# Optimization experiments

Hardware: AMD Instinct MI355X
Metric: run time of the kernel (lower is better)

## Reference

```python
import jax, jax.numpy as jnp
import numpy as np


def fwht(x):
    """Fast Walsh-Hadamard transform along last axis (n must be a power of 2).
    Loop runs log2(n) times (fixed, ~12 iters) -- fully vectorized butterflies."""
    n = x.shape[-1]
    prefix = x.shape[:-1]
    x = x.reshape(-1, n)
    h = 1
    while h < n:
        x = x.reshape(-1, n // (2 * h), 2, h)
        a, b = x[:, :, 0, :], x[:, :, 1, :]
        x = jnp.stack([a + b, a - b], axis=2).reshape(-1, n)
        h *= 2
    return x.reshape(prefix + (n,))


def setup_inputs() -> dict:
    key = jax.random.key(0)
    ks = jax.random.split(key, 8)
    Bz, S, N, M = 4, 2048, 4096, 4096   # batch, seq, in_features, out_features
    CODESZ, CB_SIZE, RANK = 8, 256, 64
    inp = {}
    inp["input"] = jax.random.normal(ks[0], (Bz, S, N), dtype=jnp.float32)
    inp["Qidxs"] = jax.random.randint(ks[1], (M, N // CODESZ), 0, CB_SIZE, dtype=jnp.int32)
    inp["codebook_vals"] = jax.random.normal(ks[2], (CB_SIZE, CODESZ), dtype=jnp.float32)
    # SU/SV are random sign vectors in QuIP#
    inp["SU"] = jnp.sign(jax.random.normal(ks[3], (N,), dtype=jnp.float32))
    inp["SV"] = jnp.sign(jax.random.normal(ks[4], (M,), dtype=jnp.float32))
    inp["Wscale"] = jnp.ones((), dtype=jnp.float32)
    inp["A"] = jax.random.normal(ks[5], (M, RANK), dtype=jnp.float32) * 0.01
    inp["B"] = jax.random.normal(ks[6], (RANK, N), dtype=jnp.float32) * 0.01
    return inp


def reference(input, Qidxs, codebook_vals, SU, SV, Wscale, A, B):
    n = SU.shape[0]   # in_features
    m = SV.shape[0]   # out_features
    lead = input.shape[:-1]
    x = input.reshape(-1, n).astype(jnp.float32)          # [T, n]
    # input rotation: x <- H^T (x * SU) / sqrt(n)   (matmul_hadUt, K=1 case)
    x = fwht(x * SU) * (1.0 / jnp.sqrt(jnp.float32(n)))
    # low-rank correction branch (rank > 0)
    Bx = x @ B.T                                          # [T, rank]
    # dequantize: codebook lookup [m, n/codesz, codesz] -> [m, n]
    W = codebook_vals[Qidxs].reshape(m, n)
    z = (x @ W.T) * Wscale                                # [T, m]
    z = z + Bx @ A.T
    # output rotation: z <- SV * (H z) / sqrt(m)
    z = fwht(z) * (1.0 / jnp.sqrt(jnp.float32(m))) * SV
    return z.reshape(lead + (m,))
```

## Files before the change

kernel.cpp:

```cpp
#include <hip/hip_runtime.h>
#include <hip/hip_bf16.h>


typedef __attribute__((ext_vector_type(8))) short short8;
typedef __attribute__((ext_vector_type(16))) float f32x16;

#define T_ROWS 8192
#define NDIM   4096
#define MDIM   4096

__device__ __forceinline__ void gld_lds16(const void* g, void* lds_uniform) {
    __builtin_amdgcn_global_load_lds(
        (const __attribute__((address_space(1))) unsigned int*)(unsigned long long)(uintptr_t)g,
        (__attribute__((address_space(3))) unsigned int*)(unsigned int)(uintptr_t)lds_uniform,
        16, 0, 0);
}

__device__ __forceinline__ void bfly(float& a, float& b) {
    float s = a + b, d = a - b; a = s; b = d;
}

__device__ __forceinline__ void fwht16(float* v) {
#pragma unroll
    for (int h = 1; h <= 8; h <<= 1)
#pragma unroll
        for (int j = 0; j < 16; ++j)
            if (!(j & h)) bfly(v[j], v[j | h]);
}

__global__ __launch_bounds__(256) void fwht_in_kernel(
        const float* __restrict__ in, const float* __restrict__ SU,
        __hip_bfloat16* __restrict__ xout) {
    __shared__ float sh[4352];
    const int t = threadIdx.x;
    const size_t r = blockIdx.x;
    float v[16];
    {
        const float4* s4 = (const float4*)(in + (r << 12) + t * 16);
        const float4* u4 = (const float4*)(SU + t * 16);
#pragma unroll
        for (int q = 0; q < 4; ++q) {
            float4 a = s4[q], u = u4[q];
            v[4 * q + 0] = a.x * u.x; v[4 * q + 1] = a.y * u.y;
            v[4 * q + 2] = a.z * u.z; v[4 * q + 3] = a.w * u.w;
        }
    }
    fwht16(v);
#pragma unroll
    for (int j = 0; j < 16; ++j) sh[17 * t + j] = v[j];
    __syncthreads();
    const int baseB = (t & 15) + 272 * (t >> 4);
#pragma unroll
    for (int j = 0; j < 16; ++j) v[j] = sh[baseB + 17 * j];
    fwht16(v);
#pragma unroll
    for (int j = 0; j < 16; ++j) sh[baseB + 17 * j] = v[j];
    __syncthreads();
    const int baseC = t + (t >> 4);
#pragma unroll
    for (int j = 0; j < 16; ++j) v[j] = sh[baseC + 272 * j];
    fwht16(v);
    __hip_bfloat16* dst = xout + (r << 12);
#pragma unroll
    for (int j = 0; j < 16; ++j)
        dst[(j << 8) + t] = __float2bfloat16(v[j] * 0.015625f);
}

__global__ __launch_bounds__(256) void fwht_out_kernel(
        float* __restrict__ z, const float* __restrict__ SV) {
    __shared__ float sh[4352];
    const int t = threadIdx.x;
    const size_t r = blockIdx.x;
    float* row = z + (r << 12);
    float v[16];
    {
        const float4* s4 = (const float4*)(row + t * 16);
#pragma unroll
        for (int q = 0; q < 4; ++q) {
            float4 a = s4[q];
            v[4 * q + 0] = a.x; v[4 * q + 1] = a.y;
            v[4 * q + 2] = a.z; v[4 * q + 3] = a.w;
        }
    }
    fwht16(v);
#pragma unroll
    for (int j = 0; j < 16; ++j) sh[17 * t + j] = v[j];
    __syncthreads();
    const int baseB = (t & 15) + 272 * (t >> 4);
#pragma unroll
    for (int j = 0; j < 16; ++j) v[j] = sh[baseB + 17 * j];
    fwht16(v);
#pragma unroll
    for (int j = 0; j < 16; ++j) sh[baseB + 17 * j] = v[j];
    __syncthreads();
    const int baseC = t + (t >> 4);
#pragma unroll
    for (int j = 0; j < 16; ++j) v[j] = sh[baseC + 272 * j];
    fwht16(v);
#pragma unroll
    for (int j = 0; j < 16; ++j)
        row[(j << 8) + t] = v[j] * 0.015625f * SV[(j << 8) + t];
}

__global__ __launch_bounds__(256) void dequant_kernel(
        const int* __restrict__ Qidxs, const float* __restrict__ cb,
        const float* __restrict__ Wscale, const float* __restrict__ A,
        const float* __restrict__ B, __hip_bfloat16* __restrict__ Weff) {
    __shared__ float At[64][68];
    __shared__ float Bs[64][68];
    __shared__ float cbs[2048];
    const int t = threadIdx.x;
    const int i0 = blockIdx.y * 64, j0 = blockIdx.x * 64;

    {
        const float* ga = A + (size_t)i0 * 64;
        const int r = t >> 2, kb = (t & 3) * 16;
#pragma unroll
        for (int j = 0; j < 16; ++j) At[kb + j][r] = ga[t * 16 + j];
        const int k = t >> 2, c0 = (t & 3) * 16;
        const float* gb = B + (size_t)k * NDIM + j0 + c0;
#pragma unroll
        for (int j = 0; j < 16; ++j) Bs[k][c0 + j] = gb[j];
#pragma unroll
        for (int j = 0; j < 8; ++j) cbs[t * 8 + j] = cb[t * 8 + j];
    }
    __syncthreads();

    const int ty = t >> 4, tx = t & 15;
    float acc[4][4];
#pragma unroll
    for (int a = 0; a < 4; ++a)
#pragma unroll
        for (int b = 0; b < 4; ++b) acc[a][b] = 0.f;

#pragma unroll 8
    for (int k = 0; k < 64; ++k) {
        const float4 av = *(const float4*)&At[k][ty * 4];
        const float4 bv = *(const float4*)&Bs[k][tx * 4];
        const float aa[4] = {av.x, av.y, av.z, av.w};
        const float bb[4] = {bv.x, bv.y, bv.z, bv.w};
#pragma unroll
        for (int ii = 0; ii < 4; ++ii)
#pragma unroll
            for (int jj = 0; jj < 4; ++jj) acc[ii][jj] += aa[ii] * bb[jj];
    }

    const float wsc = Wscale[0];
#pragma unroll
    for (int ii = 0; ii < 4; ++ii) {
        const int i = i0 + ty * 4 + ii;
        const int* qrow = Qidxs + (size_t)i * (NDIM / 8);
        union { __hip_bfloat16 h[4]; unsigned long long u; } pk;
#pragma unroll
        for (int jj = 0; jj < 4; ++jj) {
            const int j = j0 + tx * 4 + jj;
            const int idx = qrow[j >> 3];
            const float val = cbs[idx * 8 + (j & 7)] * wsc + acc[ii][jj];
            pk.h[jj] = __float2bfloat16(val);
        }
        *(unsigned long long*)&Weff[(size_t)i * NDIM + j0 + tx * 4] = pk.u;
    }
}

__global__ __launch_bounds__(512, 2) void gemm256_kernel(
        const __hip_bfloat16* __restrict__ X, const __hip_bfloat16* __restrict__ W,
        float* __restrict__ Z) {
    __shared__ short smem[65536];

    const int b = blockIdx.x;
    const int swz = (b & 7) * 64 + (b >> 3);
    const int bm = swz >> 4, bn = swz & 15;

    const int tid = threadIdx.x;
    const int lane = tid & 63, wid = tid >> 6;
    const int wm = wid >> 2, wn = wid & 3;
    const int l31 = lane & 31, kg = lane >> 5, le7 = lane & 7;
    const int rowV = l31 * 64;
    const int xr = le7 ^ ((lane >> 4) & 1);
    const int ck0 = ((2 * ((0 + 2 * wm) & 3) + kg) ^ xr) << 3;
    const int ck1 = ((2 * ((1 + 2 * wm) & 3) + kg) ^ xr) << 3;
    const int ck2 = ((2 * ((2 + 2 * wm) & 3) + kg) ^ xr) << 3;
    const int ck3 = ((2 * ((3 + 2 * wm) & 3) + kg) ^ xr) << 3;
    const int wbase = wid << 9;

    const int grow = tid >> 3;
    const int scol = (((tid & 7) ^ (grow & 7) ^ ((grow >> 4) & 3)) << 3);
    const __hip_bfloat16* gA = X + (size_t)(bm * 256 + grow) * NDIM + scol;
    const __hip_bfloat16* gB = W + (size_t)(bn * 256 + grow) * NDIM + scol;

#define STA2(OFS, H, Q, BUF) gld_lds16(gA + (size_t)(((H) * 128 + (Q) * 64) * NDIM) + (OFS), \
        &smem[(BUF) * 32768 + (H) * 8192 + (Q) * 4096 + wbase])
#define STB2(OFS, H, Q, BUF) gld_lds16(gB + (size_t)(((H) * 128 + (Q) * 64) * NDIM) + (OFS), \
        &smem[(BUF) * 32768 + 16384 + (H) * 8192 + (Q) * 4096 + wbase])
#define STAGE_A(OFS, BUF) do { STA2(OFS,0,0,BUF); STA2(OFS,0,1,BUF); \
                               STA2(OFS,1,0,BUF); STA2(OFS,1,1,BUF); } while (0)
#define STAGE_B(OFS, BUF) do { STB2(OFS,0,0,BUF); STB2(OFS,0,1,BUF); \
                               STB2(OFS,1,0,BUF); STB2(OFS,1,1,BUF); } while (0)

#define RD32_I(CK, BUF, A0,A1,A2,A3,B0,B1) do { \
    const short* aP = smem + (BUF) * 32768 + wm * 8192 + rowV; \
    const short* bP = smem + (BUF) * 32768 + 16384 + wn * 4096 + rowV; \
    A0 = *(const short8*)(aP + (CK)); \
    A1 = *(const short8*)(aP + 2048 + ((CK) ^ 16)); \
    A2 = *(const short8*)(aP + 4096 + (CK)); \
    A3 = *(const short8*)(aP + 6144 + ((CK) ^ 16)); \
    B0 = *(const short8*)(bP + (CK)); \
    B1 = *(const short8*)(bP + 2048 + ((CK) ^ 16)); \
} while (0)
#define RD32(...) RD32_I(__VA_ARGS__)

#define MM32_I(A0,A1,A2,A3,B0,B1) do { \
    c00 = __builtin_amdgcn_mfma_f32_32x32x16_bf16(A0, B0, c00, 0, 0, 0); \
    c10 = __builtin_amdgcn_mfma_f32_32x32x16_bf16(A1, B0, c10, 0, 0, 0); \
    c01 = __builtin_amdgcn_mfma_f32_32x32x16_bf16(A0, B1, c01, 0, 0, 0); \
    c11 = __builtin_amdgcn_mfma_f32_32x32x16_bf16(A1, B1, c11, 0, 0, 0); \
    c20 = __builtin_amdgcn_mfma_f32_32x32x16_bf16(A2, B0, c20, 0, 0, 0); \
    c30 = __builtin_amdgcn_mfma_f32_32x32x16_bf16(A3, B0, c30, 0, 0, 0); \
    c21 = __builtin_amdgcn_mfma_f32_32x32x16_bf16(A2, B1, c21, 0, 0, 0); \
    c31 = __builtin_amdgcn_mfma_f32_32x32x16_bf16(A3, B1, c31, 0, 0, 0); \
} while (0)
#define MM32(...) MM32_I(__VA_ARGS__)

#define SARGS0 s0a0,s0a1,s0a2,s0a3,s0b0,s0b1
#define SARGS1 s1a0,s1a1,s1a2,s1a3,s1b0,s1b1
#define SARGS2 s2a0,s2a1,s2a2,s2a3,s2b0,s2b1

#define TILE32_I(CUR, M3P, DO_ST, DO_PF, LAST, \
               SA0,SA1,SA2,SA3,SA4,SA5, SB0,SB1,SB2,SB3,SB4,SB5, \
               SC0,SC1,SC2,SC3,SC4,SC5) do { \
    if (DO_ST) { STAGE_A(64, 1 - (CUR)); STAGE_B(64, 1 - (CUR)); } \
    if (M3P) MM32(SA0,SA1,SA2,SA3,SA4,SA5);              \
    RD32(ck1, CUR, SC0,SC1,SC2,SC3,SC4,SC5); \
    MM32(SB0,SB1,SB2,SB3,SB4,SB5);                       \
    RD32(ck2, CUR, SA0,SA1,SA2,SA3,SA4,SA5); \
    MM32(SC0,SC1,SC2,SC3,SC4,SC5);                       \
    RD32(ck3, CUR, SB0,SB1,SB2,SB3,SB4,SB5); \
    MM32(SA0,SA1,SA2,SA3,SA4,SA5);                       \
    if (!(LAST)) { \
        asm volatile("s_waitcnt lgkmcnt(0)" ::: "memory"); \
        asm volatile("s_waitcnt vmcnt(0)" ::: "memory"); \
        __builtin_amdgcn_s_barrier(); \
        asm volatile("" ::: "memory"); \
    } \
    if (DO_PF) RD32(ck0, 1 - (CUR), SA0,SA1,SA2,SA3,SA4,SA5);   \
    gA += 64; gB += 64; \
} while (0)
#define TILE32(...) TILE32_I(__VA_ARGS__)

    f32x16 c00 = {0}, c01 = {0}, c10 = {0}, c11 = {0};
    f32x16 c20 = {0}, c21 = {0}, c30 = {0}, c31 = {0};
    short8 s0a0, s0a1, s0a2, s0a3, s0b0, s0b1;
    short8 s1a0, s1a1, s1a2, s1a3, s1b0, s1b1;
    short8 s2a0, s2a1, s2a2, s2a3, s2b0, s2b1;

    STAGE_A(0, 0);
    STAGE_B(0, 0);
    asm volatile("s_waitcnt vmcnt(0)" ::: "memory");
    __builtin_amdgcn_s_barrier();
    asm volatile("" ::: "memory");
    RD32(ck0, 0, SARGS1);

    TILE32(0, 0, 1, 1, 0, SARGS0, SARGS1, SARGS2);
    for (int i = 0; i < 31; ++i) {
        TILE32(1, 1, 1, 1, 0, SARGS1, SARGS0, SARGS2);
        TILE32(0, 1, 1, 1, 0, SARGS0, SARGS1, SARGS2);
    }
    TILE32(1, 1, 0, 0, 1, SARGS1, SARGS0, SARGS2);
    MM32(SARGS0);

    const size_t r0 = (size_t)bm * 256 + wm * 128 + 4 * (lane >> 5);
    const size_t cb0 = (size_t)bn * 256 + wn * 64 + l31;
#define CWR(CC, M, N) do { \
    _Pragma("unroll") \
    for (int rg = 0; rg < 16; ++rg) \
        Z[(r0 + (M) * 32 + (rg & 3) + 8 * (rg >> 2)) * MDIM + cb0 + (N) * 32] = CC[rg]; \
} while (0)
    CWR(c00, 0, 0); CWR(c01, 0, 1);
    CWR(c10, 1, 0); CWR(c11, 1, 1);
    CWR(c20, 2, 0); CWR(c21, 2, 1);
    CWR(c30, 3, 0); CWR(c31, 3, 1);
}

extern "C" void kernel_launch(void* const* d_in, const int* in_sizes, int n_in,
                              void* d_out, int out_size, void* d_ws, size_t ws_size,
                              hipStream_t stream) {
    const float* input  = (const float*)d_in[0];
    const int*   Qidxs  = (const int*)d_in[1];
    const float* cbvals = (const float*)d_in[2];
    const float* SU     = (const float*)d_in[3];
    const float* SV     = (const float*)d_in[4];
    const float* Wscale = (const float*)d_in[5];
    const float* A      = (const float*)d_in[6];
    const float* B      = (const float*)d_in[7];
    float* out = (float*)d_out;

    __hip_bfloat16* xbf = (__hip_bfloat16*)d_ws;
    __hip_bfloat16* wbf = (__hip_bfloat16*)((char*)d_ws + (size_t)T_ROWS * NDIM * 2);

    fwht_in_kernel<<<T_ROWS, 256, 0, stream>>>(input, SU, xbf);
    dequant_kernel<<<dim3(MDIM / 64, MDIM / 64), 256, 0, stream>>>(
        Qidxs, cbvals, Wscale, A, B, wbf);
    gemm256_kernel<<<(T_ROWS / 256) * (MDIM / 256), 512, 0, stream>>>(xbf, wbf, out);
    fwht_out_kernel<<<T_ROWS, 256, 0, stream>>>(out, SV);
}
```

Before: 378.4 us.

## Restructure GEMM main loop to stage B two tiles ahead with partial vmcnt waits

Rewrites the bf16 GEMM K-loop so each tile first loads all B fragments into registers, then hits a barrier and reuses the freed B buffer to prefetch B two tiles ahead, while A is prefetched one tile ahead. The end-of-tile wait becomes a partial vmcnt so the newest B loads stay in flight across the barrier. The per-warp rotated chunk order in the LDS reads is replaced by a fixed order. The aim is deeper overlap of global loads with MFMA work, at the cost of an extra barrier per tile, more live registers, and possibly more LDS bank conflicts from the simpler chunk order.

```diff
diff --git a/kernel.cpp b/kernel.cpp
--- a/kernel.cpp
+++ b/kernel.cpp
@@ -177,10 +177,10 @@
     const int l31 = lane & 31, kg = lane >> 5, le7 = lane & 7;
     const int rowV = l31 * 64;
     const int xr = le7 ^ ((lane >> 4) & 1);
-    const int ck0 = ((2 * ((0 + 2 * wm) & 3) + kg) ^ xr) << 3;
-    const int ck1 = ((2 * ((1 + 2 * wm) & 3) + kg) ^ xr) << 3;
-    const int ck2 = ((2 * ((2 + 2 * wm) & 3) + kg) ^ xr) << 3;
-    const int ck3 = ((2 * ((3 + 2 * wm) & 3) + kg) ^ xr) << 3;
+    const int ck0 = ((0 + kg) ^ xr) << 3;
+    const int ck1 = ((2 + kg) ^ xr) << 3;
+    const int ck2 = ((4 + kg) ^ xr) << 3;
+    const int ck3 = ((6 + kg) ^ xr) << 3;
     const int wbase = wid << 9;
 
     const int grow = tid >> 3;
@@ -197,19 +197,14 @@
 #define STAGE_B(OFS, BUF) do { STB2(OFS,0,0,BUF); STB2(OFS,0,1,BUF); \
                                STB2(OFS,1,0,BUF); STB2(OFS,1,1,BUF); } while (0)
 
-#define RD32_I(CK, BUF, A0,A1,A2,A3,B0,B1) do { \
-    const short* aP = smem + (BUF) * 32768 + wm * 8192 + rowV; \
-    const short* bP = smem + (BUF) * 32768 + 16384 + wn * 4096 + rowV; \
+#define RA(CK, A0,A1,A2,A3) do { \
     A0 = *(const short8*)(aP + (CK)); \
     A1 = *(const short8*)(aP + 2048 + ((CK) ^ 16)); \
     A2 = *(const short8*)(aP + 4096 + (CK)); \
     A3 = *(const short8*)(aP + 6144 + ((CK) ^ 16)); \
-    B0 = *(const short8*)(bP + (CK)); \
-    B1 = *(const short8*)(bP + 2048 + ((CK) ^ 16)); \
 } while (0)
-#define RD32(...) RD32_I(__VA_ARGS__)
-
-#define MM32_I(A0,A1,A2,A3,B0,B1) do { \
+
+#define MM32(A0,A1,A2,A3,B0,B1) do { \
     c00 = __builtin_amdgcn_mfma_f32_32x32x16_bf16(A0, B0, c00, 0, 0, 0); \
     c10 = __builtin_amdgcn_mfma_f32_32x32x16_bf16(A1, B0, c10, 0, 0, 0); \
     c01 = __builtin_amdgcn_mfma_f32_32x32x16_bf16(A0, B1, c01, 0, 0, 0); \
@@ -219,54 +214,58 @@
     c21 = __builtin_amdgcn_mfma_f32_32x32x16_bf16(A2, B1, c21, 0, 0, 0); \
     c31 = __builtin_amdgcn_mfma_f32_32x32x16_bf16(A3, B1, c31, 0, 0, 0); \
 } while (0)
-#define MM32(...) MM32_I(__VA_ARGS__)
-
-#define SARGS0 s0a0,s0a1,s0a2,s0a3,s0b0,s0b1
-#define SARGS1 s1a0,s1a1,s1a2,s1a3,s1b0,s1b1
-#define SARGS2 s2a0,s2a1,s2a2,s2a3,s2b0,s2b1
-
-#define TILE32_I(CUR, M3P, DO_ST, DO_PF, LAST, \
-               SA0,SA1,SA2,SA3,SA4,SA5, SB0,SB1,SB2,SB3,SB4,SB5, \
-               SC0,SC1,SC2,SC3,SC4,SC5) do { \
-    if (DO_ST) { STAGE_A(64, 1 - (CUR)); STAGE_B(64, 1 - (CUR)); } \
-    if (M3P) MM32(SA0,SA1,SA2,SA3,SA4,SA5);              \
-    RD32(ck1, CUR, SC0,SC1,SC2,SC3,SC4,SC5); \
-    MM32(SB0,SB1,SB2,SB3,SB4,SB5);                       \
-    RD32(ck2, CUR, SA0,SA1,SA2,SA3,SA4,SA5); \
-    MM32(SC0,SC1,SC2,SC3,SC4,SC5);                       \
-    RD32(ck3, CUR, SB0,SB1,SB2,SB3,SB4,SB5); \
-    MM32(SA0,SA1,SA2,SA3,SA4,SA5);                       \
+
+#define TILE(CUR, DO_STA, DO_STB, VMEND, LAST) do { \
+    const short* aP = smem + (CUR) * 32768 + wm * 8192 + rowV; \
+    const short* bP = smem + (CUR) * 32768 + 16384 + wn * 4096 + rowV; \
+    short8 b00, b01, b10, b11, b20, b21, b30, b31; \
+    short8 sa0, sa1, sa2, sa3, ta0, ta1, ta2, ta3; \
+    b00 = *(const short8*)(bP + ck0); \
+    b01 = *(const short8*)(bP + 2048 + (ck0 ^ 16)); \
+    b10 = *(const short8*)(bP + ck1); \
+    b11 = *(const short8*)(bP + 2048 + (ck1 ^ 16)); \
+    b20 = *(const short8*)(bP + ck2); \
+    b21 = *(const short8*)(bP + 2048 + (ck2 ^ 16)); \
+    b30 = *(const short8*)(bP + ck3); \
+    b31 = *(const short8*)(bP + 2048 + (ck3 ^ 16)); \
+    asm volatile("s_waitcnt lgkmcnt(0)" ::: "memory"); \
+    __builtin_amdgcn_s_barrier();                     \
+    asm volatile("" ::: "memory"); \
+    if (DO_STA) STAGE_A(64, 1 - (CUR)); \
+    if (DO_STB) STAGE_B(128, (CUR)); \
+    RA(ck0, sa0, sa1, sa2, sa3); \
+    RA(ck1, ta0, ta1, ta2, ta3); \
+    MM32(sa0, sa1, sa2, sa3, b00, b01);               \
+    RA(ck2, sa0, sa1, sa2, sa3); \
+    MM32(ta0, ta1, ta2, ta3, b10, b11);               \
+    RA(ck3, ta0, ta1, ta2, ta3); \
+    MM32(sa0, sa1, sa2, sa3, b20, b21);               \
+    MM32(ta0, ta1, ta2, ta3, b30, b31);               \
     if (!(LAST)) { \
         asm volatile("s_waitcnt lgkmcnt(0)" ::: "memory"); \
-        asm volatile("s_waitcnt vmcnt(0)" ::: "memory"); \
+        asm volatile("s_waitcnt vmcnt(" #VMEND ")" ::: "memory"); \
         __builtin_amdgcn_s_barrier(); \
         asm volatile("" ::: "memory"); \
     } \
-    if (DO_PF) RD32(ck0, 1 - (CUR), SA0,SA1,SA2,SA3,SA4,SA5);   \
     gA += 64; gB += 64; \
 } while (0)
-#define TILE32(...) TILE32_I(__VA_ARGS__)
 
     f32x16 c00 = {0}, c01 = {0}, c10 = {0}, c11 = {0};
     f32x16 c20 = {0}, c21 = {0}, c30 = {0}, c31 = {0};
-    short8 s0a0, s0a1, s0a2, s0a3, s0b0, s0b1;
-    short8 s1a0, s1a1, s1a2, s1a3, s1b0, s1b1;
-    short8 s2a0, s2a1, s2a2, s2a3, s2b0, s2b1;
 
     STAGE_A(0, 0);
     STAGE_B(0, 0);
+    STAGE_B(64, 1);
     asm volatile("s_waitcnt vmcnt(0)" ::: "memory");
     __builtin_amdgcn_s_barrier();
     asm volatile("" ::: "memory");
-    RD32(ck0, 0, SARGS1);
-
-    TILE32(0, 0, 1, 1, 0, SARGS0, SARGS1, SARGS2);
+
     for (int i = 0; i < 31; ++i) {
-        TILE32(1, 1, 1, 1, 0, SARGS1, SARGS0, SARGS2);
-        TILE32(0, 1, 1, 1, 0, SARGS0, SARGS1, SARGS2);
-    }
-    TILE32(1, 1, 0, 0, 1, SARGS1, SARGS0, SARGS2);
-    MM32(SARGS0);
+        TILE(0, 1, 1, 4, 0);
+        TILE(1, 1, 1, 4, 0);
+    }
+    TILE(0, 1, 0, 0, 0);
+    TILE(1, 0, 0, 0, 1);
 
     const size_t r0 = (size_t)bm * 256 + wm * 128 + 4 * (lane >> 5);
     const size_t cb0 = (size_t)bn * 256 + wn * 64 + l31;
```

After: 385.6 us. About the same (+1.9%).
